# Kernel tuning notes

Measured on AMD Instinct MI355X. Metric: run time of the kernel, lower is better.

Reference implementation:

```python
import jax, jax.numpy as jnp
import numpy as np

WIN = (8, 8)          # window height/width -> seq_len n = 64
GAMMA = 16            # channel groups (s)
BLOCKS = 1024         # num_blocks == number of windows w
GATE_DIM = 256        # dim // chunks
EPS = 1e-5


def _rel_indices(win):
    # Quadratic relative-position features [n, n, 3] = (dx, dy, dx^2+dy^2)
    w, h = win
    ind = np.arange(h)[None, :] - np.arange(w)[:, None]            # (w, h)
    indx = np.tile(ind, (h, w))                                    # (n, n)
    indy = np.repeat(np.repeat(ind, h, axis=0), w, axis=1).T       # (n, n)
    indd = indx ** 2 + indy ** 2
    return jnp.asarray(np.stack([indx, indy, indd], axis=-1), dtype=jnp.float32)


def setup_inputs() -> dict:
    key = jax.random.key(0)
    k0, k1, k2 = jax.random.split(key, 3)
    b = 4
    n = WIN[0] * WIN[1]
    return {
        "x": jax.random.normal(k0, (b, BLOCKS, n, 2 * GATE_DIM), dtype=jnp.float32),
        "norm_weight": jnp.ones((GATE_DIM,), jnp.float32),
        "norm_bias": jnp.zeros((GATE_DIM,), jnp.float32),
        "attention_centers": 0.01 * jax.random.normal(k1, (BLOCKS * GAMMA, 2), jnp.float32),
        "attention_spreads": 1.0 + 0.01 * jax.random.normal(k2, (BLOCKS * GAMMA,), jnp.float32),
        "token_proj_n_bias": jnp.zeros((BLOCKS, n, 1), jnp.float32),
    }


def reference(x, norm_weight, norm_bias, attention_centers, attention_spreads, token_proj_n_bias):
    b, w, n, d = x.shape
    # chunk into gate halves: u mixed spatially, v is the gate
    u, v = jnp.split(x, 2, axis=-1)                                # [b,w,n,gd] each
    # LayerNorm over channel dim (biased variance, as torch)
    mean = u.mean(-1, keepdims=True)
    var = u.var(-1, keepdims=True)
    u = (u - mean) * jax.lax.rsqrt(var + EPS) * norm_weight + norm_bias
    # quadratic positional weights (QuaMap.forward_qua_pos)
    mu1, mu2 = attention_centers[:, 0], attention_centers[:, 1]
    a = attention_spreads ** 2
    pos_proj = jnp.stack([a * mu1, a * mu2, -0.5 * jnp.ones_like(mu1)], axis=-1)  # [g*w, 3]
    rel = _rel_indices(WIN)                                        # [n,n,3]
    pos_score = jnp.einsum('mnd,bd->bmn', rel, pos_proj)           # [g*w, n, n]
    win_weight = jax.nn.softmax(pos_score, axis=-1)
    # rearrange '(s b) m n -> b m n s' with s=gamma
    win_weight = win_weight.reshape(GAMMA, w, n, n).transpose(1, 2, 3, 0)  # [w,m,n,s]
    # rearrange 'b w n (v s) -> b w n v s'
    vdim = u.shape[-1] // GAMMA
    uu = u.reshape(b, w, n, vdim, GAMMA)
    # windowed spatial mixing + per-window bias
    mixed = jnp.einsum('wmns,bwnvs->bwmvs', win_weight, uu)
    mixed = mixed + token_proj_n_bias[None, :, :, None, :]          # [1,w,n,1,1]
    u = mixed.reshape(b, w, n, vdim * GAMMA)
    return u * v
```

## Files before the change

kernel.cpp:

```cpp
#include <hip/hip_runtime.h>
#include <cstdint>

#if __has_builtin(__builtin_amdgcn_exp2f)
#define EXP2F(x) __builtin_amdgcn_exp2f(x)
#else
#define EXP2F(x) exp2f(x)
#endif

typedef _Float16 half8 __attribute__((ext_vector_type(8)));
typedef float    f32x4 __attribute__((ext_vector_type(4)));


__global__ __launch_bounds__(512, 6) void sgating_kernel(
    const float* __restrict__ x,
    const float* __restrict__ norm_w,
    const float* __restrict__ norm_b,
    const float* __restrict__ centers,
    const float* __restrict__ spreads,
    const float* __restrict__ tbias,
    float* __restrict__ out)
{
    __shared__ __align__(16) float smem[8192];
    _Float16* Us = (_Float16*)smem;

    const int t     = threadIdx.x;
    const int wv    = t >> 6;
    const int lane  = t & 63;
    const int bw    = blockIdx.x;
    const int w_idx = bw & 1023;
    const size_t xbase = (size_t)bw * (64 * 512);

    {
        const float4 w4 = *(const float4*)(norm_w + lane * 4);
        const float4 b4 = *(const float4*)(norm_b + lane * 4);
        half8 uar[4];
#pragma unroll
        for (int r = 0; r < 8; ++r) {
            const int n = wv * 8 + r;
            const float4 u = *(const float4*)(x + xbase + (size_t)n * 512 + lane * 4);
            float s  = u.x + u.y + u.z + u.w;
            float sq = u.x*u.x + u.y*u.y + u.z*u.z + u.w*u.w;
#pragma unroll
            for (int off = 1; off < 64; off <<= 1) {
                s  += __shfl_xor(s, off);
                sq += __shfl_xor(sq, off);
            }
            const float mean = s * (1.0f/256.0f);
            const float var  = sq * (1.0f/256.0f) - mean*mean;
            const float rstd = rsqrtf(var + 1e-5f);
            uar[0][r] = (_Float16)((u.x - mean)*rstd*w4.x + b4.x);
            uar[1][r] = (_Float16)((u.y - mean)*rstd*w4.y + b4.y);
            uar[2][r] = (_Float16)((u.z - mean)*rstd*w4.z + b4.z);
            uar[3][r] = (_Float16)((u.w - mean)*rstd*w4.w + b4.w);
        }
#pragma unroll
        for (int j = 0; j < 4; ++j) {
            const int d  = lane * 4 + j;
            const int s  = d & 15;
            const int vd = d >> 4;
            const int nb = wv ^ (vd & 7);
            *(half8*)(Us + (s << 10) + (vd << 6) + (nb << 3)) = uar[j];
        }
    }
    __syncthreads();

    const int vd16 = lane & 15;
    const int g    = lane >> 4;
    const float LOG2E = 1.4426950408889634f;
    const float C2    = 0.72134752044448f;

    float bias4[4];
#pragma unroll
    for (int nt = 0; nt < 4; ++nt)
        bias4[nt] = tbias[w_idx * 64 + nt * 16 + vd16];

    const float mx  = (float)(vd16 & 7);
    const float myb = (float)(vd16 >> 3);

    f32x4 vals[2][4];

#pragma unroll
    for (int hh = 0; hh < 2; ++hh) {
        const int s  = wv + 8 * hh;
        const int hb = (s << 10) | w_idx;
        float a = spreads[hb]; a *= a;
        const float axl = a * centers[2*hb + 0] * LOG2E;
        const float ayl = a * centers[2*hb + 1] * LOG2E;

        half8 ua[2];
#pragma unroll
        for (int kt = 0; kt < 2; ++kt) {
            const int nb = (g + 4*kt) ^ (vd16 & 7);
            ua[kt] = *(const half8*)(Us + (s << 10) + (vd16 << 6) + (nb << 3));
        }

        float ex[8];
        float sx = 0.f;
#pragma unroll
        for (int j = 0; j < 8; ++j) {
            const float dx = (float)j - mx;
            ex[j] = EXP2F(dx * fmaf(-C2, dx, axl));
            sx += ex[j];
        }

        f32x4 acc[4];
        float rs[4];
#pragma unroll
        for (int nt = 0; nt < 4; ++nt) {
            acc[nt] = (f32x4){0.f,0.f,0.f,0.f};
            rs[nt] = 0.f;
        }

#pragma unroll
        for (int nt = 0; nt < 4; ++nt) {
            const float my = (float)(2*nt) + myb;
#pragma unroll
            for (int kt = 0; kt < 2; ++kt) {
                const float dy  = my - (float)(g + 4*kt);
                const float eyv = EXP2F(dy * fmaf(-C2, dy, ayl));
                rs[nt] += eyv;
                half8 wb;
#pragma unroll
                for (int j = 0; j < 8; ++j)
                    wb[j] = (_Float16)(ex[j] * eyv);
                acc[nt] = __builtin_amdgcn_mfma_f32_16x16x32_f16(ua[kt], wb, acc[nt], 0, 0, 0);
            }
        }

#pragma unroll
        for (int nt = 0; nt < 4; ++nt) {
            float r = rs[nt] * sx;
            r += __shfl_xor(r, 16);
            r += __shfl_xor(r, 32);
            const float inv = 1.0f / r;
#pragma unroll
            for (int j = 0; j < 4; ++j)
                vals[hh][nt][j] = acc[nt][j] * inv + bias4[nt];
        }
    }

    __syncthreads();

    const size_t obase = (size_t)bw * (64 * 256);
#pragma unroll
    for (int h = 0; h < 2; ++h) {
#pragma unroll
        for (int hh = 0; hh < 2; ++hh) {
            const int s = wv + 8 * hh;
#pragma unroll
            for (int q = 0; q < 2; ++q) {
                const int nt  = 2*h + q;
                const int m   = nt * 16 + vd16;
                const int col = (s * 16 + g * 4) ^ ((m & 7) << 2);
                *(f32x4*)(smem + ((m & 31) << 8) + col) = vals[hh][nt];
            }
        }
        __syncthreads();

#pragma unroll
        for (int k = 0; k < 4; ++k) {
            const int flat = (t << 2) + (k << 11);
            const int mr = flat >> 8;
            const int m  = mr + 32 * h;
            const int c  = flat & 255;
            const int vd = c >> 4;
            const int s0 = c & 15;
            const int sw = (m & 7) << 2;
            float4 mxv;
            mxv.x = smem[(mr << 8) + ((((s0 + 0) << 4) + vd) ^ sw)];
            mxv.y = smem[(mr << 8) + ((((s0 + 1) << 4) + vd) ^ sw)];
            mxv.z = smem[(mr << 8) + ((((s0 + 2) << 4) + vd) ^ sw)];
            mxv.w = smem[(mr << 8) + ((((s0 + 3) << 4) + vd) ^ sw)];
            const float4 vv = *(const float4*)(x + xbase + (size_t)m * 512 + 256 + c);
            float4 o;
            o.x = mxv.x * vv.x; o.y = mxv.y * vv.y;
            o.z = mxv.z * vv.z; o.w = mxv.w * vv.w;
            *(float4*)(out + obase + (m << 8) + c) = o;
        }
        if (h == 0) __syncthreads();
    }
}

extern "C" void kernel_launch(void* const* d_in, const int* in_sizes, int n_in,
                              void* d_out, int out_size, void* d_ws, size_t ws_size,
                              hipStream_t stream) {
    const float* x       = (const float*)d_in[0];
    const float* norm_w  = (const float*)d_in[1];
    const float* norm_b  = (const float*)d_in[2];
    const float* centers = (const float*)d_in[3];
    const float* spreads = (const float*)d_in[4];
    const float* tbias   = (const float*)d_in[5];
    float* out = (float*)d_out;

    const int nbw = in_sizes[0] / (64 * 512);
    hipLaunchKernelGGL(sgating_kernel, dim3(nbw), dim3(512), 0, stream,
                       x, norm_w, norm_b, centers, spreads, tbias, out);
}
```

Baseline: 159.0 us.

## Interleave per-quarter MFMA mixing with gated output stores using dedicated LDS buffer

Restructures the mixing phase to compute one 16-row quarter at a time for both channel groups, and overlaps it with the gating and global stores of the previous quarter. The staging buffer for the output transpose now lives in its own LDS region, so the U tile does not have to be retired before the stores start. The x-direction exponentials are precomputed once in fp16 and multiplied in fp16 to build the MFMA weights. In exchange, LDS use rises from 32 KB to 48 KB per block, which may lower how many blocks fit per CU. Doing the weight products in half precision also slightly reduces accuracy.

```diff
diff --git a/kernel.cpp b/kernel.cpp
--- a/kernel.cpp
+++ b/kernel.cpp
@@ -20,8 +20,9 @@
     const float* __restrict__ tbias,
     float* __restrict__ out)
 {
-    __shared__ __align__(16) float smem[8192];
+    __shared__ __align__(16) float smem[12288];
     _Float16* Us = (_Float16*)smem;
+    float*    Qm = smem + 8192;
 
     const int t     = threadIdx.x;
     const int wv    = t >> 6;
@@ -29,6 +30,7 @@
     const int bw    = blockIdx.x;
     const int w_idx = bw & 1023;
     const size_t xbase = (size_t)bw * (64 * 512);
+    const size_t obase = (size_t)bw * (64 * 256);
 
     {
         const float4 w4 = *(const float4*)(norm_w + lane * 4);
@@ -64,120 +66,118 @@
     }
     __syncthreads();
 
-    const int vd16 = lane & 15;
-    const int g    = lane >> 4;
+    const int m16 = lane & 15;
+    const int g   = lane >> 4;
     const float LOG2E = 1.4426950408889634f;
     const float C2    = 0.72134752044448f;
+    const float mx  = (float)(m16 & 7);
+    const float myb = (float)(m16 >> 3);
+
+    const int sA = wv, sB = wv + 8;
 
     float bias4[4];
 #pragma unroll
     for (int nt = 0; nt < 4; ++nt)
-        bias4[nt] = tbias[w_idx * 64 + nt * 16 + vd16];
+        bias4[nt] = tbias[w_idx * 64 + nt * 16 + m16];
 
-    const float mx  = (float)(vd16 & 7);
-    const float myb = (float)(vd16 >> 3);
-
-    f32x4 vals[2][4];
-
-#pragma unroll
-    for (int hh = 0; hh < 2; ++hh) {
-        const int s  = wv + 8 * hh;
-        const int hb = (s << 10) | w_idx;
-        float a = spreads[hb]; a *= a;
-        const float axl = a * centers[2*hb + 0] * LOG2E;
-        const float ayl = a * centers[2*hb + 1] * LOG2E;
-
-        half8 ua[2];
-#pragma unroll
-        for (int kt = 0; kt < 2; ++kt) {
-            const int nb = (g + 4*kt) ^ (vd16 & 7);
-            ua[kt] = *(const half8*)(Us + (s << 10) + (vd16 << 6) + (nb << 3));
-        }
-
-        float ex[8];
-        float sx = 0.f;
+    float aylA, aylB, sxA, sxB;
+    half8 exhA, exhB;
+    {
+        const int hbA = (sA << 10) | w_idx;
+        const int hbB = (sB << 10) | w_idx;
+        float aq = spreads[hbA]; aq *= aq;
+        const float axlA = aq * centers[2*hbA] * LOG2E;
+        aylA = aq * centers[2*hbA + 1] * LOG2E;
+        aq = spreads[hbB]; aq *= aq;
+        const float axlB = aq * centers[2*hbB] * LOG2E;
+        aylB = aq * centers[2*hbB + 1] * LOG2E;
+        sxA = 0.f; sxB = 0.f;
 #pragma unroll
         for (int j = 0; j < 8; ++j) {
             const float dx = (float)j - mx;
-            ex[j] = EXP2F(dx * fmaf(-C2, dx, axl));
-            sx += ex[j];
-        }
-
-        f32x4 acc[4];
-        float rs[4];
-#pragma unroll
-        for (int nt = 0; nt < 4; ++nt) {
-            acc[nt] = (f32x4){0.f,0.f,0.f,0.f};
-            rs[nt] = 0.f;
-        }
-
-#pragma unroll
-        for (int nt = 0; nt < 4; ++nt) {
-            const float my = (float)(2*nt) + myb;
-#pragma unroll
-            for (int kt = 0; kt < 2; ++kt) {
-                const float dy  = my - (float)(g + 4*kt);
-                const float eyv = EXP2F(dy * fmaf(-C2, dy, ayl));
-                rs[nt] += eyv;
-                half8 wb;
-#pragma unroll
-                for (int j = 0; j < 8; ++j)
-                    wb[j] = (_Float16)(ex[j] * eyv);
-                acc[nt] = __builtin_amdgcn_mfma_f32_16x16x32_f16(ua[kt], wb, acc[nt], 0, 0, 0);
-            }
-        }
-
-#pragma unroll
-        for (int nt = 0; nt < 4; ++nt) {
-            float r = rs[nt] * sx;
-            r += __shfl_xor(r, 16);
-            r += __shfl_xor(r, 32);
-            const float inv = 1.0f / r;
-#pragma unroll
-            for (int j = 0; j < 4; ++j)
-                vals[hh][nt][j] = acc[nt][j] * inv + bias4[nt];
+            const float eA = EXP2F(dx * fmaf(-C2, dx, axlA));
+            const float eB = EXP2F(dx * fmaf(-C2, dx, axlB));
+            sxA += eA; sxB += eB;
+            exhA[j] = (_Float16)eA;
+            exhB[j] = (_Float16)eB;
         }
     }
 
-    __syncthreads();
+    auto compute_quarter = [&](int nt, f32x4& vOutA, f32x4& vOutB) {
+        const float my = (float)(2*nt) + myb;
+        f32x4 aA = (f32x4){0.f,0.f,0.f,0.f};
+        f32x4 aB = (f32x4){0.f,0.f,0.f,0.f};
+        float rsA = 0.f, rsB = 0.f;
+#pragma unroll
+        for (int kt = 0; kt < 2; ++kt) {
+            const int nb = (g + 4*kt) ^ (m16 & 7);
+            const half8 uA = *(const half8*)(Us + (sA << 10) + (m16 << 6) + (nb << 3));
+            const half8 uB = *(const half8*)(Us + (sB << 10) + (m16 << 6) + (nb << 3));
+            const float dy  = my - (float)(g + 4*kt);
+            const float eA = EXP2F(dy * fmaf(-C2, dy, aylA));
+            const float eB = EXP2F(dy * fmaf(-C2, dy, aylB));
+            rsA += eA; rsB += eB;
+            const _Float16 ehA = (_Float16)eA;
+            const _Float16 ehB = (_Float16)eB;
+            half8 wA, wB;
+#pragma unroll
+            for (int j = 0; j < 8; ++j) {
+                wA[j] = exhA[j] * ehA;
+                wB[j] = exhB[j] * ehB;
+            }
+            aA = __builtin_amdgcn_mfma_f32_16x16x32_f16(uA, wA, aA, 0, 0, 0);
+            aB = __builtin_amdgcn_mfma_f32_16x16x32_f16(uB, wB, aB, 0, 0, 0);
+        }
+        float rA = rsA * sxA;
+        rA += __shfl_xor(rA, 16); rA += __shfl_xor(rA, 32);
+        float rB = rsB * sxB;
+        rB += __shfl_xor(rB, 16); rB += __shfl_xor(rB, 32);
+        const float iA = 1.0f / rA;
+        const float iB = 1.0f / rB;
+        const float bm = bias4[nt];
+#pragma unroll
+        for (int j = 0; j < 4; ++j) {
+            vOutA[j] = aA[j] * iA + bm;
+            vOutB[j] = aB[j] * iB + bm;
+        }
+    };
 
-    const size_t obase = (size_t)bw * (64 * 256);
+    f32x4 vA, vB, nA, nB;
+    compute_quarter(0, vA, vB);
+
 #pragma unroll
-    for (int h = 0; h < 2; ++h) {
-#pragma unroll
-        for (int hh = 0; hh < 2; ++hh) {
-            const int s = wv + 8 * hh;
-#pragma unroll
-            for (int q = 0; q < 2; ++q) {
-                const int nt  = 2*h + q;
-                const int m   = nt * 16 + vd16;
-                const int col = (s * 16 + g * 4) ^ ((m & 7) << 2);
-                *(f32x4*)(smem + ((m & 31) << 8) + col) = vals[hh][nt];
-            }
-        }
+    for (int nt = 0; nt < 4; ++nt) {
+        const int swz = (m16 & 7) << 2;
+        *(f32x4*)(Qm + (m16 << 8) + ((sA * 16 + g * 4) ^ swz)) = vA;
+        *(f32x4*)(Qm + (m16 << 8) + ((sB * 16 + g * 4) ^ swz)) = vB;
         __syncthreads();
 
+        if (nt < 3) compute_quarter(nt + 1, nA, nB);
+
 #pragma unroll
-        for (int k = 0; k < 4; ++k) {
-            const int flat = (t << 2) + (k << 11);
-            const int mr = flat >> 8;
-            const int m  = mr + 32 * h;
-            const int c  = flat & 255;
-            const int vd = c >> 4;
-            const int s0 = c & 15;
-            const int sw = (m & 7) << 2;
+        for (int k = 0; k < 2; ++k) {
+            const int mr = wv + 8 * k;
+            const int m  = nt * 16 + mr;
+            const int c4 = lane * 4;
+            const int vd = c4 >> 4;
+            const int s0 = c4 & 15;
+            const int sw2 = (m & 7) << 2;
             float4 mxv;
-            mxv.x = smem[(mr << 8) + ((((s0 + 0) << 4) + vd) ^ sw)];
-            mxv.y = smem[(mr << 8) + ((((s0 + 1) << 4) + vd) ^ sw)];
-            mxv.z = smem[(mr << 8) + ((((s0 + 2) << 4) + vd) ^ sw)];
-            mxv.w = smem[(mr << 8) + ((((s0 + 3) << 4) + vd) ^ sw)];
-            const float4 vv = *(const float4*)(x + xbase + (size_t)m * 512 + 256 + c);
+            mxv.x = Qm[(mr << 8) + ((((s0 + 0) << 4) + vd) ^ sw2)];
+            mxv.y = Qm[(mr << 8) + ((((s0 + 1) << 4) + vd) ^ sw2)];
+            mxv.z = Qm[(mr << 8) + ((((s0 + 2) << 4) + vd) ^ sw2)];
+            mxv.w = Qm[(mr << 8) + ((((s0 + 3) << 4) + vd) ^ sw2)];
+            const float4 vv = *(const float4*)(x + xbase + (size_t)m * 512 + 256 + c4);
             float4 o;
             o.x = mxv.x * vv.x; o.y = mxv.y * vv.y;
             o.z = mxv.z * vv.z; o.w = mxv.w * vv.w;
-            *(float4*)(out + obase + (m << 8) + c) = o;
+            *(float4*)(out + obase + m * 256 + c4) = o;
         }
-        if (h == 0) __syncthreads();
+
+        if (nt < 3) {
+            __syncthreads();
+            vA = nA; vB = nB;
+        }
     }
 }
 
```

Result: no change. 157.5 us (-0.9%).
